# Kernel tuning notes

Hardware: AMD Instinct MI355X
Metric: run time of the kernel (lower is better)

The kernel has to match this reference:

```python
import jax, jax.numpy as jnp
import numpy as np

N = 768
INPUT_DIM = 128
HIDDEN = 256
HEADS = 8
HEAD_DIM = HIDDEN // HEADS  # 32
SCALE = float(np.sqrt(HEAD_DIM))


def _linear_params(key, fan_in, fan_out):
    kw, kb = jax.random.split(key)
    lim = 1.0 / np.sqrt(fan_in)
    W = jax.random.uniform(kw, (fan_in, fan_out), jnp.float32, -lim, lim)
    b = jax.random.uniform(kb, (fan_out,), jnp.float32, -lim, lim)
    return W, b


def setup_inputs() -> dict:
    key = jax.random.key(0)
    ks = jax.random.split(key, 9)
    x = jax.random.normal(ks[0], (N, INPUT_DIM), jnp.float32)
    pos = jax.random.normal(ks[1], (N, 3), jnp.float32)
    Wq, bq = _linear_params(ks[2], INPUT_DIM, HIDDEN)
    Wk, bk = _linear_params(ks[3], INPUT_DIM, HIDDEN)
    Wv, bv = _linear_params(ks[4], INPUT_DIM, HIDDEN)
    Wo, bo = _linear_params(ks[5], HIDDEN, HIDDEN)
    W1, b1 = _linear_params(ks[6], 3, HIDDEN)
    W2, b2 = _linear_params(ks[7], HIDDEN, HIDDEN)
    W3, b3 = _linear_params(ks[8], HIDDEN, HEAD_DIM)
    return dict(x=x, pos=pos, Wq=Wq, bq=bq, Wk=Wk, bk=bk, Wv=Wv, bv=bv,
                Wo=Wo, bo=bo, W1=W1, b1=b1, W2=W2, b2=b2, W3=W3, b3=b3)


def reference(x, pos, Wq, bq, Wk, bk, Wv, bv, Wo, bo, W1, b1, W2, b2, W3, b3):
    n = x.shape[0]
    Q = (x @ Wq + bq).reshape(n, HEADS, HEAD_DIM)
    K = (x @ Wk + bk).reshape(n, HEADS, HEAD_DIM)
    V = (x @ Wv + bv).reshape(n, HEADS, HEAD_DIM)

    # rel_pos[i, j] = pos[j] - pos[i], shape (N, N, 3)
    rel = pos[None, :, :] - pos[:, None, :]
    h = jax.nn.relu(rel @ W1 + b1)          # (N, N, HIDDEN)
    h = jax.nn.relu(h @ W2 + b2)            # (N, N, HIDDEN)
    enc = h @ W3 + b3                        # (N, N, HEAD_DIM)

    scores = jnp.einsum('ihd,jhd->hij', Q, K) / SCALE
    scores = scores + jnp.einsum('ihd,ijd->hij', Q, enc) / SCALE
    attn = jax.nn.softmax(scores, axis=-1)   # (H, N, N); dropout is identity at eval
    out = jnp.einsum('hij,jhd->ihd', attn, V).reshape(n, HIDDEN)
    return out @ Wo + bo
```

## Files before the change

### kernel.cpp

```cpp
#include <hip/hip_runtime.h>
#include <hip/hip_bf16.h>

#define N 768
#define IN_DIM 128
#define HID 256
#define HD 32
#define TJ 64
#define NT (N / TJ)
#define SCALE_INV 0.17677669529663687f

typedef short s16x8 __attribute__((ext_vector_type(8)));
typedef float f32x4 __attribute__((ext_vector_type(4)));

__device__ __forceinline__ float bf2f(unsigned short s) {
    return __uint_as_float(((unsigned)s) << 16);
}
__device__ __forceinline__ unsigned short bf_bits(float f) {
    __hip_bfloat16 h = __float2bfloat16(f);
    union { __hip_bfloat16 h; unsigned short u; } c; c.h = h; return c.u;
}
__device__ __forceinline__ unsigned cvt2(float a, float b) {
    __hip_bfloat162 h2 = __float22bfloat162_rn(make_float2(a, b));
    union { __hip_bfloat162 h; unsigned u; } c; c.h = h2; return c.u;
}

#define BAR_LDS() do { asm volatile("s_waitcnt lgkmcnt(0)" ::: "memory"); \
                       __builtin_amdgcn_s_barrier(); } while (0)

__global__ __launch_bounds__(256) void prep_kernel(
    const float* __restrict__ x, const float* __restrict__ pos,
    const float* __restrict__ Wq, const float* __restrict__ bq,
    const float* __restrict__ Wk, const float* __restrict__ bk,
    const float* __restrict__ Wv, const float* __restrict__ bv,
    const float* __restrict__ W1, const float* __restrict__ W2,
    const float* __restrict__ W3, const float* __restrict__ Wo,
    float* __restrict__ Q, float* __restrict__ Kt,
    unsigned short* __restrict__ Vt, float* __restrict__ A,
    unsigned short* __restrict__ w2f, float* __restrict__ WoT,
    unsigned short* __restrict__ w3qg)
{
    const int bx = blockIdx.x, t = threadIdx.x;
    __shared__ float xs[IN_DIM];
    __shared__ float ps[3];
    __shared__ float qrow[HID];

    if (bx >= N) {
        const int p = (bx - N) * 256 + t;
        const int e = p & 7, l = (p >> 3) & 63, nt = (p >> 9) & 15, s = p >> 13;
        const int krow = 32 * s + 8 * (l >> 4) + e;
        const int ncol = 16 * nt + (l & 15);
        w2f[p] = bf_bits(W2[krow * HID + ncol]);
        WoT[p] = Wo[(p & 255) * HID + (p >> 8)];
        return;
    }

    const int i = bx;
    if (t < IN_DIM) xs[t] = x[i * IN_DIM + t];
    if (t < 3) ps[t] = pos[i * 3 + t];
    __syncthreads();
    float q = bq[t], k = bk[t], v = bv[t];
#pragma unroll 8
    for (int kk = 0; kk < IN_DIM; ++kk) {
        const float xv = xs[kk];
        q += xv * Wq[kk * HID + t];
        k += xv * Wk[kk * HID + t];
        v += xv * Wv[kk * HID + t];
    }
    const float a = ps[0] * W1[t] + ps[1] * W1[HID + t] + ps[2] * W1[2 * HID + t];
    Q[i * HID + t] = q;
    Kt[(size_t)t * N + i] = k;
    Vt[(size_t)t * N + i] = bf_bits(v);
    A[i * HID + t] = a;
    qrow[t] = q;
    __syncthreads();

    const int l = t & 63, sp = t >> 6, lg = l >> 4, hh = l & 15;
#pragma unroll
    for (int ss = 0; ss < 2; ++ss) {
        const int s = 2 * sp + ss;
        s16x8 frag = {0, 0, 0, 0, 0, 0, 0, 0};
        if (hh < 8) {
#pragma unroll
            for (int e = 0; e < 8; ++e) {
                const int kk = 32 * s + 8 * lg + e;
                const float* w3p = W3 + kk * HD;
                float acc = 0.f;
#pragma unroll
                for (int d0 = 0; d0 < 32; d0 += 4) {
                    const float4 wv = *(const float4*)(w3p + d0);
                    acc += wv.x * qrow[hh * HD + d0] + wv.y * qrow[hh * HD + d0 + 1]
                         + wv.z * qrow[hh * HD + d0 + 2] + wv.w * qrow[hh * HD + d0 + 3];
                }
                frag[e] = (short)bf_bits(acc);
            }
        }
        *(s16x8*)(w3qg + (size_t)i * 4096 + (size_t)(s * 64 + l) * 8) = frag;
    }
}

__global__ __launch_bounds__(256) void s1_kernel(
    const float* __restrict__ Q, const float* __restrict__ Kt,
    float* __restrict__ S1)
{
    const int t = threadIdx.x;
    const int i0 = (blockIdx.x / 12) * 32;
    const int j0 = (blockIdx.x % 12) * 64;
    __shared__ float qTs[256 * 36];

    {
        const int iq = t & 31;
        const int dbase = (t >> 5) * 32;
        const int xk = t >> 5;
        const int colsw = (((iq >> 2) ^ xk) << 2) + (iq & 3);
        const float* qp = Q + (size_t)(i0 + iq) * HID + dbase;
#pragma unroll
        for (int cc = 0; cc < 8; ++cc) {
            const float4 qv = *(const float4*)(qp + 4 * cc);
            qTs[(dbase + 4 * cc + 0) * 36 + colsw] = qv.x;
            qTs[(dbase + 4 * cc + 1) * 36 + colsw] = qv.y;
            qTs[(dbase + 4 * cc + 2) * 36 + colsw] = qv.z;
            qTs[(dbase + 4 * cc + 3) * 36 + colsw] = qv.w;
        }
    }
    __syncthreads();

    const int h = t >> 5, jj = t & 31;
    const int j1 = j0 + jj, j2 = j0 + jj + 32;
    f32x4 acc0[8] = {}, acc1[8] = {};
    const float* kp = Kt + (size_t)(32 * h) * N + j1;
#pragma unroll 4
    for (int d = 0; d < 32; ++d) {
        const float k0 = kp[(size_t)d * N];
        const float k1 = kp[(size_t)d * N + 32];
        const float* qrow = &qTs[(32 * h + d) * 36];
#pragma unroll
        for (int ic = 0; ic < 8; ++ic) {
            const f32x4 qv = *(const f32x4*)&qrow[(ic ^ h) << 2];
            acc0[ic] += qv * k0;
            acc1[ic] += qv * k1;
        }
    }
    float* op = S1 + (size_t)h * (N * N) + (size_t)i0 * N;
#pragma unroll
    for (int ic = 0; ic < 8; ++ic)
#pragma unroll
        for (int u = 0; u < 4; ++u) {
            op[(size_t)(4 * ic + u) * N + j1] = acc0[ic][u];
            op[(size_t)(4 * ic + u) * N + j2] = acc1[ic][u];
        }
}

__global__ __launch_bounds__(256, 2) void fused_main_kernel(
    const float* __restrict__ Ag, const float* __restrict__ S1,
    const unsigned short* __restrict__ Vt,
    const unsigned short* __restrict__ w2fg, const unsigned short* __restrict__ w3qg,
    const float* __restrict__ b1, const float* __restrict__ b2,
    const float* __restrict__ WoT, const float* __restrict__ bo,
    float* __restrict__ out)
{
    const int i = blockIdx.x, t = threadIdx.x;
    const int w = t >> 6, l = t & 63;
    const int lg = l >> 4, l15 = l & 15;

    __shared__ __align__(16) short h1f[4 * 8 * 64 * 8];
    __shared__ __align__(16) short h2s[64 * 264];
    __shared__ __align__(16) short w3qf[8 * 64 * 8];
    __shared__ __align__(16) float slds[8 * 68];
    __shared__ __align__(16) float plds[8 * 68];
    __shared__ float basek[HID];
    __shared__ float oa[HID];
    __shared__ float hm[8], hpsum[8], hresc[8];

    basek[t] = b1[t] - Ag[(size_t)i * HID + t];
    {
        const int c0 = t, c1 = t + 256;
        *(s16x8*)&w3qf[c0 * 8] = *(const s16x8*)(w3qg + (size_t)i * 4096 + (size_t)c0 * 8);
        *(s16x8*)&w3qf[c1 * 8] = *(const s16x8*)(w3qg + (size_t)i * 4096 + (size_t)c1 * 8);
    }
    if (t < 8) { hm[t] = -3.0e38f; hpsum[t] = 0.f; }
    float bias[4];
#pragma unroll
    for (int n = 0; n < 4; ++n) bias[n] = b2[64 * w + 16 * n + l15];

    float pv = 0.f;
    const int h = t >> 5;
    const unsigned short* vrow = Vt + (size_t)t * N;
    BAR_LDS();

#pragma unroll 1
    for (int tile = 0; tile < NT; ++tile) {
        const int j0 = tile * TJ;

        const int jj = 16 * w + l15;
        const float* ap = Ag + (size_t)(j0 + jj) * HID + 8 * lg;
#pragma unroll
        for (int s = 0; s < 8; ++s) {
            const float4 a0 = *(const float4*)(ap + 32 * s);
            const float4 a1 = *(const float4*)(ap + 32 * s + 4);
            const float4 c0 = *(const float4*)&basek[32 * s + 8 * lg];
            const float4 c4 = *(const float4*)&basek[32 * s + 8 * lg + 4];
            uint4 hv;
            hv.x = cvt2(fmaxf(a0.x + c0.x, 0.f), fmaxf(a0.y + c0.y, 0.f));
            hv.y = cvt2(fmaxf(a0.z + c0.z, 0.f), fmaxf(a0.w + c0.w, 0.f));
            hv.z = cvt2(fmaxf(a1.x + c4.x, 0.f), fmaxf(a1.y + c4.y, 0.f));
            hv.w = cvt2(fmaxf(a1.z + c4.z, 0.f), fmaxf(a1.w + c4.w, 0.f));
            *(uint4*)&h1f[((w * 8 + s) * 64 + l) * 8] = hv;
        }
        s16x8 bfr[32];
#pragma unroll
        for (int s = 0; s < 8; ++s)
#pragma unroll
            for (int n = 0; n < 4; ++n)
                bfr[s * 4 + n] = *(const s16x8*)(w2fg +
                    (size_t)(((s * 16 + 4 * w + n) * 64 + l)) * 8);
        BAR_LDS();

#pragma unroll
        for (int mt = 0; mt < 4; ++mt) {
            s16x8 a[8];
#pragma unroll
            for (int s = 0; s < 8; ++s)
                a[s] = *(const s16x8*)&h1f[((mt * 8 + s) * 64 + l) * 8];
#pragma unroll
            for (int n = 0; n < 4; ++n) {
                f32x4 acc = {bias[n], bias[n], bias[n], bias[n]};
#pragma unroll
                for (int s = 0; s < 8; ++s)
                    acc = __builtin_amdgcn_mfma_f32_16x16x32_bf16(a[s], bfr[s * 4 + n], acc, 0, 0, 0);
                const int col = 64 * w + 16 * n + l15;
                const int jrow = 16 * mt + 4 * lg;
#pragma unroll
                for (int r = 0; r < 4; ++r)
                    h2s[(jrow + r) * 264 + col] = (short)bf_bits(fmaxf(acc[r], 0.f));
            }
        }
        BAR_LDS();

        float4 s1v = make_float4(0.f, 0.f, 0.f, 0.f);
        if (l15 < 8)
            s1v = *(const float4*)(S1 + (size_t)l15 * (N * N) + (size_t)i * N
                                   + j0 + 16 * w + 4 * lg);
        f32x4 acc2 = {};
#pragma unroll
        for (int s = 0; s < 8; ++s) {
            const s16x8 a2 = *(const s16x8*)&h2s[(16 * w + l15) * 264 + 32 * s + 8 * lg];
            const s16x8 wq = *(const s16x8*)&w3qf[(s * 64 + l) * 8];
            acc2 = __builtin_amdgcn_mfma_f32_16x16x32_bf16(a2, wq, acc2, 0, 0, 0);
        }
        if (l15 < 8) {
            float4 sc;
            sc.x = (acc2[0] + s1v.x) * SCALE_INV;
            sc.y = (acc2[1] + s1v.y) * SCALE_INV;
            sc.z = (acc2[2] + s1v.z) * SCALE_INV;
            sc.w = (acc2[3] + s1v.w) * SCALE_INV;
            *(float4*)&slds[l15 * 68 + 16 * w + 4 * lg] = sc;
        }
        BAR_LDS();

        {
            const int h0 = w, h1 = w + 4;
            const float s0 = slds[h0 * 68 + l];
            const float s1 = slds[h1 * 68 + l];
            float m0 = s0, m1 = s1;
#pragma unroll
            for (int o = 1; o < 64; o <<= 1) {
                m0 = fmaxf(m0, __shfl_xor(m0, o));
                m1 = fmaxf(m1, __shfl_xor(m1, o));
            }
            const float M0 = hm[h0], M1 = hm[h1];
            const float nm0 = fmaxf(M0, m0), nm1 = fmaxf(M1, m1);
            const float p0 = __expf(s0 - nm0), p1 = __expf(s1 - nm1);
            plds[h0 * 68 + l] = p0;
            plds[h1 * 68 + l] = p1;
            float t0 = p0, t1 = p1;
#pragma unroll
            for (int o = 1; o < 64; o <<= 1) {
                t0 += __shfl_xor(t0, o);
                t1 += __shfl_xor(t1, o);
            }
            if (l == 0) {
                const float r0 = __expf(M0 - nm0), r1 = __expf(M1 - nm1);
                hresc[h0] = r0; hresc[h1] = r1;
                hpsum[h0] = hpsum[h0] * r0 + t0;
                hpsum[h1] = hpsum[h1] * r1 + t1;
                hm[h0] = nm0; hm[h1] = nm1;
            }
        }
        BAR_LDS();

        {
            pv *= hresc[h];
            const unsigned short* vp = vrow + j0;
            const float* pp = &plds[h * 68];
#pragma unroll
            for (int c = 0; c < 8; ++c) {
                const s16x8 vv = *(const s16x8*)(vp + c * 8);
                const float4 pa = *(const float4*)(pp + 8 * c);
                const float4 pb = *(const float4*)(pp + 8 * c + 4);
                pv += pa.x * bf2f((unsigned short)vv[0]) + pa.y * bf2f((unsigned short)vv[1])
                    + pa.z * bf2f((unsigned short)vv[2]) + pa.w * bf2f((unsigned short)vv[3])
                    + pb.x * bf2f((unsigned short)vv[4]) + pb.y * bf2f((unsigned short)vv[5])
                    + pb.z * bf2f((unsigned short)vv[6]) + pb.w * bf2f((unsigned short)vv[7]);
            }
        }
    }

    oa[t] = pv / hpsum[h];
    BAR_LDS();
    float r = bo[t];
    const float* wop = WoT + (size_t)t * HID;
#pragma unroll 4
    for (int k = 0; k < HID; k += 4) {
        const float4 ov = *(const float4*)&oa[k];
        const float4 wv = *(const float4*)(wop + k);
        r += ov.x * wv.x + ov.y * wv.y + ov.z * wv.z + ov.w * wv.w;
    }
    out[(size_t)i * HID + t] = r;
}

extern "C" void kernel_launch(void* const* d_in, const int* in_sizes, int n_in,
                              void* d_out, int out_size, void* d_ws, size_t ws_size,
                              hipStream_t stream)
{
    const float* x   = (const float*)d_in[0];
    const float* pos = (const float*)d_in[1];
    const float* Wq  = (const float*)d_in[2];
    const float* bq  = (const float*)d_in[3];
    const float* Wk  = (const float*)d_in[4];
    const float* bk  = (const float*)d_in[5];
    const float* Wv  = (const float*)d_in[6];
    const float* bv  = (const float*)d_in[7];
    const float* Wo  = (const float*)d_in[8];
    const float* bo  = (const float*)d_in[9];
    const float* W1  = (const float*)d_in[10];
    const float* b1  = (const float*)d_in[11];
    const float* W2  = (const float*)d_in[12];
    const float* b2  = (const float*)d_in[13];
    const float* W3  = (const float*)d_in[14];
    const float* b3  = (const float*)d_in[15];
    (void)b3;
    float* out = (float*)d_out;

    char* ws = (char*)d_ws;
    float* Q  = (float*)(ws + 0);
    float* A  = (float*)(ws + 786432);
    float* Kt = (float*)(ws + 1572864);
    unsigned short* Vtb = (unsigned short*)(ws + 2359296);
    float* S1 = (float*)(ws + 2752512);
    unsigned short* w2f  = (unsigned short*)(ws + 21626880);
    unsigned short* w3qg = (unsigned short*)(ws + 21757952);
    float* WoT = (float*)(ws + 28049408);

    prep_kernel<<<1024, 256, 0, stream>>>(x, pos, Wq, bq, Wk, bk, Wv, bv,
                                          W1, W2, W3, Wo,
                                          Q, Kt, Vtb, A, w2f, WoT, w3qg);
    s1_kernel<<<288, 256, 0, stream>>>(Q, Kt, S1);
    fused_main_kernel<<<N, 256, 0, stream>>>(A, S1, Vtb, w2f, w3qg,
                                             b1, b2, WoT, bo, out);
}
```

Before: 227.7 us.

## Split attention key range across two blocks per row with a combine kernel

The main fused kernel now launches two blocks per query row, each covering half of the key tiles. Each block writes its unnormalized PV accumulator, per-head running max and partial softmax sum to workspace. A new combine kernel merges the two halves with max-rescaling, normalizes, and applies the output projection. The aim is to double the grid so it fills the GPU's CUs better and reduces the tail of a partial last wave. The cost is duplicated per-block setup, an extra launch and extra global traffic for the partial results.

```diff
diff --git a/kernel.cpp b/kernel.cpp
--- a/kernel.cpp
+++ b/kernel.cpp
@@ -7,6 +7,7 @@
 #define HD 32
 #define TJ 64
 #define NT (N / TJ)
+#define NTH (NT / 2)
 #define SCALE_INV 0.17677669529663687f
 
 typedef short s16x8 __attribute__((ext_vector_type(8)));
@@ -155,10 +156,12 @@
     const unsigned short* __restrict__ Vt,
     const unsigned short* __restrict__ w2fg, const unsigned short* __restrict__ w3qg,
     const float* __restrict__ b1, const float* __restrict__ b2,
-    const float* __restrict__ WoT, const float* __restrict__ bo,
-    float* __restrict__ out)
-{
-    const int i = blockIdx.x, t = threadIdx.x;
+    float* __restrict__ pv0g, float* __restrict__ pv1g,
+    float* __restrict__ psump, float* __restrict__ mp)
+{
+    const int bid = blockIdx.x;
+    const int i = bid >> 1, jh = bid & 1;
+    const int t = threadIdx.x;
     const int w = t >> 6, l = t & 63;
     const int lg = l >> 4, l15 = l & 15;
 
@@ -168,7 +171,6 @@
     __shared__ __align__(16) float slds[8 * 68];
     __shared__ __align__(16) float plds[8 * 68];
     __shared__ float basek[HID];
-    __shared__ float oa[HID];
     __shared__ float hm[8], hpsum[8], hresc[8];
 
     basek[t] = b1[t] - Ag[(size_t)i * HID + t];
@@ -188,8 +190,8 @@
     BAR_LDS();
 
 #pragma unroll 1
-    for (int tile = 0; tile < NT; ++tile) {
-        const int j0 = tile * TJ;
+    for (int tt = 0; tt < NTH; ++tt) {
+        const int j0 = (jh * NTH + tt) * TJ;
 
         const int jj = 16 * w + l15;
         const float* ap = Ag + (size_t)(j0 + jj) * HID + 8 * lg;
@@ -305,8 +307,34 @@
         }
     }
 
-    oa[t] = pv / hpsum[h];
-    BAR_LDS();
+    float* pvb = jh ? pv1g : pv0g;
+    pvb[(size_t)i * HID + t] = pv;
+    if (t < 8) {
+        psump[(size_t)bid * 8 + t] = hpsum[t];
+        mp[(size_t)bid * 8 + t] = hm[t];
+    }
+}
+
+__global__ __launch_bounds__(256) void combine_kernel(
+    const float* __restrict__ pv0g, const float* __restrict__ pv1g,
+    const float* __restrict__ psump, const float* __restrict__ mp,
+    const float* __restrict__ WoT, const float* __restrict__ bo,
+    float* __restrict__ out)
+{
+    const int i = blockIdx.x, t = threadIdx.x;
+    const int h = t >> 5;
+    __shared__ float oa[HID];
+
+    const float m0 = mp[(size_t)(2 * i) * 8 + h];
+    const float m1 = mp[(size_t)(2 * i + 1) * 8 + h];
+    const float ms = fmaxf(m0, m1);
+    const float e0 = __expf(m0 - ms), e1 = __expf(m1 - ms);
+    const float num = pv0g[(size_t)i * HID + t] * e0 + pv1g[(size_t)i * HID + t] * e1;
+    const float den = psump[(size_t)(2 * i) * 8 + h] * e0
+                    + psump[(size_t)(2 * i + 1) * 8 + h] * e1;
+    oa[t] = num / den;
+    __syncthreads();
+
     float r = bo[t];
     const float* wop = WoT + (size_t)t * HID;
 #pragma unroll 4
@@ -350,11 +378,16 @@
     unsigned short* w2f  = (unsigned short*)(ws + 21626880);
     unsigned short* w3qg = (unsigned short*)(ws + 21757952);
     float* WoT = (float*)(ws + 28049408);
+    float* pv0g  = (float*)(ws + 0);
+    float* pv1g  = (float*)(ws + 1572864);
+    float* psump = (float*)(ws + 28311552);
+    float* mp    = (float*)(ws + 28360704);
 
     prep_kernel<<<1024, 256, 0, stream>>>(x, pos, Wq, bq, Wk, bk, Wv, bv,
                                           W1, W2, W3, Wo,
                                           Q, Kt, Vtb, A, w2f, WoT, w3qg);
     s1_kernel<<<288, 256, 0, stream>>>(Q, Kt, S1);
-    fused_main_kernel<<<N, 256, 0, stream>>>(A, S1, Vtb, w2f, w3qg,
-                                             b1, b2, WoT, bo, out);
-}
+    fused_main_kernel<<<2 * N, 256, 0, stream>>>(A, S1, Vtb, w2f, w3qg,
+                                                 b1, b2, pv0g, pv1g, psump, mp);
+    combine_kernel<<<N, 256, 0, stream>>>(pv0g, pv1g, psump, mp, WoT, bo, out);
+}
```

New measurement: 211.9 us. 1.07x faster.
